# Kernel tuning notes

Hardware: AMD Instinct MI355X
Metric: run time of the kernel (lower is better)

## Reference

```python
import jax, jax.numpy as jnp
import numpy as np

WSCALE = 0.05  # keep ReLU MLP activations in a sane range


def setup_inputs() -> dict:
    key = jax.random.key(0)
    ks = jax.random.split(key, 9)
    B, D, H = 2048, 64, 512
    return {
        "x": jax.random.normal(ks[0], (B, D), dtype=jnp.float32),
        "W1": jax.random.normal(ks[1], (H, D), dtype=jnp.float32) * WSCALE,
        "b1": jax.random.normal(ks[2], (H,), dtype=jnp.float32) * WSCALE,
        "W2": jax.random.normal(ks[3], (H, H), dtype=jnp.float32) * WSCALE,
        "b2": jax.random.normal(ks[4], (H,), dtype=jnp.float32) * WSCALE,
        "W3": jax.random.normal(ks[5], (H, H), dtype=jnp.float32) * WSCALE,
        "b3": jax.random.normal(ks[6], (H,), dtype=jnp.float32) * WSCALE,
        "W4": jax.random.normal(ks[7], (D, H), dtype=jnp.float32) * WSCALE,
        "b4": jax.random.normal(ks[8], (D,), dtype=jnp.float32) * WSCALE,
    }


def reference(x, W1, b1, W2, b2, W3, b3, W4, b4):
    # Score network: ReLU MLP (weights stored PyTorch-style [out, in]).
    a1 = x @ W1.T + b1          # [B, H]
    h1 = jax.nn.relu(a1)
    a2 = h1 @ W2.T + b2
    h2 = jax.nn.relu(a2)
    a3 = h2 @ W3.T + b3
    h3 = jax.nn.relu(a3)
    s = h3 @ W4.T + b4          # [B, D] score

    # Divergence = trace of Jacobian ds/dx per sample.
    # Per-sample J = W4 @ diag(m3) @ W3 @ diag(m2) @ W2 @ diag(m1) @ W1,
    # with m_k = 1[a_k > 0] (ReLU derivative; 0 at 0 like torch autograd).
    m1 = (a1 > 0).astype(x.dtype)
    m2 = (a2 > 0).astype(x.dtype)
    m3 = (a3 > 0).astype(x.dtype)
    T = m1[:, :, None] * W1[None, :, :]                 # [B, H, D]
    T = m2[:, :, None] * jnp.einsum('ij,bjd->bid', W2, T)  # [B, H, D]
    T = m3[:, :, None] * jnp.einsum('ij,bjd->bid', W3, T)  # [B, H, D]
    div = jnp.einsum('dj,bjd->b', W4, T)                # trace of J, [B]

    # Hyvarinen score: 0.5 * ||s||^2 + div
    val = 0.5 * jnp.sum(s * s, axis=1) + div
    return val
```

## Files before the change

kernel.cpp:

```cpp
#include <hip/hip_runtime.h>
#include <stdint.h>


typedef __attribute__((ext_vector_type(8))) short short8;
typedef __attribute__((ext_vector_type(4))) float f32x4;

union U16x8 {
  uint4 u;
  short8 s;
};

__device__ __forceinline__ uint16_t f2bf(float f) {
  uint32_t u = __float_as_uint(f);
  uint32_t lsb = (u >> 16) & 1u;
  u += 0x7FFFu + lsb;
  return (uint16_t)(u >> 16);
}

__device__ __forceinline__ void lds_load16(const uint4* gsrc, uint4* ldst) {
  __builtin_amdgcn_global_load_lds(
      (const __attribute__((address_space(1))) void*)gsrc,
      (__attribute__((address_space(3))) void*)ldst, 16, 0, 0);
}

__global__ __launch_bounds__(256) void convert_kernel(
    const float* __restrict__ W1, const float* __restrict__ W2,
    const float* __restrict__ W3, const float* __restrict__ W4,
    uint16_t* __restrict__ A2swz, uint16_t* __restrict__ A3swz,
    uint16_t* __restrict__ B1swz, uint16_t* __restrict__ B4swz,
    float* __restrict__ W2Tf, float* __restrict__ W3Tf,
    float* __restrict__ W1Tf, float* __restrict__ W4Tf) {
  const int i = blockIdx.x * 256 + threadIdx.x;
  if (i < 262144) {
    const int e = i;
    const int f = e >> 3, j = e & 7;
    const int lane = f & 63, fk = f >> 6;
    const int kc = fk & 15, r16 = fk >> 4;
    const int l15 = lane & 15, quad = lane >> 4;
    const int row = r16 * 16 + l15, col = kc * 32 + quad * 8 + j;
    A2swz[e] = f2bf(W2[row * 512 + col]);
  } else if (i < 524288) {
    const int e = i - 262144;
    const int f = e >> 3, j = e & 7;
    const int lane = f & 63, fk = f >> 6;
    const int kc = fk & 15, r16 = fk >> 4;
    const int l15 = lane & 15, quad = lane >> 4;
    const int row = r16 * 16 + l15, col = kc * 32 + quad * 8 + j;
    A3swz[e] = f2bf(W3[col * 512 + row]);
  } else if (i < 557056) {
    const int e = i - 524288;
    const int f = e >> 3, j = e & 7;
    const int lane = f & 63, fk = f >> 6;
    const int kc = fk >> 2, jt = fk & 3;
    const int l15 = lane & 15, quad = lane >> 4;
    const int d = jt * 16 + l15, col = kc * 32 + quad * 8 + j;
    B1swz[e] = f2bf(W1[col * 64 + d]);
  } else if (i < 589824) {
    const int e = i - 557056;
    const int f = e >> 3, j = e & 7;
    const int lane = f & 63, fk = f >> 6;
    const int kc = fk >> 2, jt = fk & 3;
    const int l15 = lane & 15, quad = lane >> 4;
    const int d = jt * 16 + l15, col = kc * 32 + quad * 8 + j;
    B4swz[e] = f2bf(W4[d * 512 + col]);
  } else if (i < 851968) {
    const int e = i - 589824;
    const int k = e >> 9, jj = e & 511;
    W2Tf[e] = W2[jj * 512 + k];
  } else if (i < 1114112) {
    const int e = i - 851968;
    const int k = e >> 9, jj = e & 511;
    W3Tf[e] = W3[jj * 512 + k];
  } else if (i < 1146880) {
    const int e = i - 1114112;
    const int k = e >> 9, jj = e & 511;
    W1Tf[e] = W1[jj * 64 + k];
  } else if (i < 1179648) {
    const int e = i - 1146880;
    const int k = e >> 6, d = e & 63;
    W4Tf[e] = W4[d * 512 + k];
  }
}

__device__ __forceinline__ void relu_store_mask4(
    float acc[4], float (*hdst)[4], uint32_t* __restrict__ mbase,
    int t, int lane, int wv) {
#pragma unroll
  for (int s = 0; s < 4; ++s) {
    const unsigned long long bal = __ballot(acc[s] > 0.f);
    if (lane == 0) {
      uint2 w2;
      w2.x = (uint32_t)bal;
      w2.y = (uint32_t)(bal >> 32);
      *(uint2*)(mbase + (size_t)s * 16 + 2 * wv) = w2;
    }
  }
  float4 r;
  r.x = acc[0] > 0.f ? acc[0] : 0.f;
  r.y = acc[1] > 0.f ? acc[1] : 0.f;
  r.z = acc[2] > 0.f ? acc[2] : 0.f;
  r.w = acc[3] > 0.f ? acc[3] : 0.f;
  *(float4*)&hdst[t][0] = r;
}

__device__ __forceinline__ void fwd_layer(
    const float* __restrict__ WT, const float* __restrict__ bias,
    const float (* __restrict__ src)[4], float (* __restrict__ dst)[4],
    uint32_t* __restrict__ mbase, int t, int lane, int wv, int K) {
  float acc[4];
  {
    const float bj = bias[t];
    acc[0] = bj; acc[1] = bj; acc[2] = bj; acc[3] = bj;
  }
  const float* Wp = WT + t;
  float wA[8], wB[8];
#pragma unroll
  for (int j = 0; j < 8; ++j) wA[j] = Wp[(size_t)j * 512];
#pragma unroll 1
  for (int kb = 0; kb < K; kb += 16) {
#pragma unroll
    for (int j = 0; j < 8; ++j) wB[j] = Wp[(size_t)(kb + 8 + j) * 512];
#pragma unroll
    for (int j = 0; j < 8; ++j) {
      const float4 h = *(const float4*)&src[kb + j][0];
      const float w = wA[j];
      acc[0] = fmaf(w, h.x, acc[0]); acc[1] = fmaf(w, h.y, acc[1]);
      acc[2] = fmaf(w, h.z, acc[2]); acc[3] = fmaf(w, h.w, acc[3]);
    }
    if (kb + 16 < K) {
#pragma unroll
      for (int j = 0; j < 8; ++j) wA[j] = Wp[(size_t)(kb + 16 + j) * 512];
    }
#pragma unroll
    for (int j = 0; j < 8; ++j) {
      const float4 h = *(const float4*)&src[kb + 8 + j][0];
      const float w = wB[j];
      acc[0] = fmaf(w, h.x, acc[0]); acc[1] = fmaf(w, h.y, acc[1]);
      acc[2] = fmaf(w, h.z, acc[2]); acc[3] = fmaf(w, h.w, acc[3]);
    }
  }
  relu_store_mask4(acc, dst, mbase, t, lane, wv);
}

__global__ __launch_bounds__(512) void forward_kernel(
    const float* __restrict__ x,
    const float* __restrict__ W1Tf, const float* __restrict__ b1,
    const float* __restrict__ W2Tf, const float* __restrict__ b2,
    const float* __restrict__ W3Tf, const float* __restrict__ b3,
    const float* __restrict__ W4Tf, const float* __restrict__ b4,
    uint32_t* __restrict__ m1p, uint32_t* __restrict__ m2p,
    uint32_t* __restrict__ m3p, float* __restrict__ out) {
  __shared__ float xs[64][4];
  __shared__ float hA[512][4];
  __shared__ float hB[512][4];
  __shared__ float p4[4][2][64];
  const int t = threadIdx.x;
  const int lane = t & 63, wv = t >> 6;
  const int b0 = blockIdx.x * 4;

  if (t < 256) {
    const int k = t >> 2, s = t & 3;
    xs[k][s] = x[(size_t)(b0 + s) * 64 + k];
  }
  __syncthreads();

  fwd_layer(W1Tf, b1, xs, hA, m1p + (size_t)b0 * 16, t, lane, wv, 64);
  __syncthreads();
  fwd_layer(W2Tf, b2, hA, hB, m2p + (size_t)b0 * 16, t, lane, wv, 512);
  __syncthreads();
  fwd_layer(W3Tf, b3, hB, hA, m3p + (size_t)b0 * 16, t, lane, wv, 512);
  __syncthreads();

  {
    const int s = wv & 3, hh = wv >> 2, d = lane;
    const int k0 = hh * 256;
    const float* Wp = W4Tf + (size_t)k0 * 64 + d;
    float ap[4] = {0.f, 0.f, 0.f, 0.f};
    float wA[8], wB[8];
#pragma unroll
    for (int j = 0; j < 8; ++j) wA[j] = Wp[(size_t)j * 64];
#pragma unroll 1
    for (int kb = 0; kb < 256; kb += 16) {
#pragma unroll
      for (int j = 0; j < 8; ++j) wB[j] = Wp[(size_t)(kb + 8 + j) * 64];
#pragma unroll
      for (int j = 0; j < 8; ++j)
        ap[j & 3] = fmaf(wA[j], hA[k0 + kb + j][s], ap[j & 3]);
      if (kb + 16 < 256) {
#pragma unroll
        for (int j = 0; j < 8; ++j) wA[j] = Wp[(size_t)(kb + 16 + j) * 64];
      }
#pragma unroll
      for (int j = 0; j < 8; ++j)
        ap[j & 3] = fmaf(wB[j], hA[k0 + kb + 8 + j][s], ap[j & 3]);
    }
    p4[s][hh][d] = (ap[0] + ap[1]) + (ap[2] + ap[3]);
  }
  __syncthreads();
  if (wv < 4) {
    const int s = wv, d = lane;
    const float a4 = p4[s][0][d] + p4[s][1][d] + b4[d];
    float sq = a4 * a4;
#pragma unroll
    for (int off = 32; off; off >>= 1) sq += __shfl_down(sq, off, 64);
    if (lane == 0) out[b0 + s] = 0.5f * sq;
  }
}

__device__ __forceinline__ void expand_mask(uint32_t byte8, uint32_t mk[4]) {
#pragma unroll
  for (int i = 0; i < 4; ++i) {
    mk[i] = (((byte8 >> (2 * i)) & 1u) ? 0x0000FFFFu : 0u) |
            (((byte8 >> (2 * i + 1)) & 1u) ? 0xFFFF0000u : 0u);
  }
}

__global__ __launch_bounds__(256, 2) void div_kernel(
    const uint4* __restrict__ A2swz, const uint4* __restrict__ A3swz,
    const uint4* __restrict__ B1swz, const uint4* __restrict__ B4swz,
    const uint32_t* __restrict__ m1p, const uint32_t* __restrict__ m2p,
    const uint32_t* __restrict__ m3p, float* __restrict__ out) {
  __shared__ uint4 sfrag[3][16][64];
  __shared__ uint32_t smask[4][2][16];
  const int t = threadIdx.x;
  const int lane = t & 63, wv = t >> 6;
  const int quad = lane >> 4;
  const int g4 = blockIdx.x;
  const int rowB0 = blockIdx.y * 64;
  const int b = g4 * 4 + wv;
  const int r16b = blockIdx.y * 4;

  const uint4* sb = (wv == 0) ? A2swz : (wv == 1) ? A3swz : (wv == 2) ? B1swz : B4swz;

  f32x4 accC[4][4], accG[4][4];
#pragma unroll
  for (int it = 0; it < 4; ++it)
#pragma unroll
    for (int jt = 0; jt < 4; ++jt) {
      accC[it][jt] = (f32x4){0.f, 0.f, 0.f, 0.f};
      accG[it][jt] = (f32x4){0.f, 0.f, 0.f, 0.f};
    }

  {
    const uint32_t* m1w = m1p + (size_t)b * 16;
    const uint32_t* m3w = m3p + (size_t)b * 16;
    if (lane < 16) smask[wv][0][lane] = m1w[lane];
    else if (lane < 32) smask[wv][1][lane & 15] = m3w[lane & 15];
  }

  auto stage = [&](int sbuf, int kc) {
#pragma unroll
    for (int q = 0; q < 4; ++q) {
      const size_t off = (wv < 2)
          ? ((size_t)((r16b + q) * 16 + kc) * 64 + lane)
          : ((size_t)(kc * 4 + q) * 64 + lane);
      lds_load16(sb + off, &sfrag[sbuf][wv * 4 + q][0]);
    }
  };

  stage(0, 0);
  stage(1, 1);
  __builtin_amdgcn_sched_barrier(0);
  asm volatile("s_waitcnt vmcnt(4)" ::: "memory");
  __builtin_amdgcn_s_barrier();
  __builtin_amdgcn_sched_barrier(0);

#pragma unroll 1
  for (int kc = 0; kc < 16; ++kc) {
    const int rb = kc % 3;
    if (kc < 14) stage((kc + 2) % 3, kc + 2);

    {
      const uint32_t m1d = __builtin_amdgcn_readfirstlane(smask[wv][0][kc]);
      uint32_t mk1[4];
      expand_mask((m1d >> (quad * 8)) & 0xFFu, mk1);

      uint4 a2[4], u1[4];
#pragma unroll
      for (int q = 0; q < 4; ++q) {
        a2[q] = sfrag[rb][q][lane];
        u1[q] = sfrag[rb][8 + q][lane];
      }
      short8 bC[4];
#pragma unroll
      for (int jt = 0; jt < 4; ++jt) {
        U16x8 u;
        u.u = u1[jt];
        u.u.x &= mk1[0]; u.u.y &= mk1[1]; u.u.z &= mk1[2]; u.u.w &= mk1[3];
        bC[jt] = u.s;
      }
      __builtin_amdgcn_s_setprio(1);
#pragma unroll
      for (int it = 0; it < 4; ++it) {
        U16x8 ua;
        ua.u = a2[it];
        const short8 af = ua.s;
#pragma unroll
        for (int jt = 0; jt < 4; ++jt)
          accC[it][jt] = __builtin_amdgcn_mfma_f32_16x16x32_bf16(af, bC[jt], accC[it][jt], 0, 0, 0);
      }
      __builtin_amdgcn_s_setprio(0);
    }

    {
      const uint32_t m3d = __builtin_amdgcn_readfirstlane(smask[wv][1][kc]);
      uint32_t mk3[4];
      expand_mask((m3d >> (quad * 8)) & 0xFFu, mk3);

      uint4 a3[4], u4[4];
#pragma unroll
      for (int q = 0; q < 4; ++q) {
        a3[q] = sfrag[rb][4 + q][lane];
        u4[q] = sfrag[rb][12 + q][lane];
      }
      short8 bG[4];
#pragma unroll
      for (int jt = 0; jt < 4; ++jt) {
        U16x8 u;
        u.u = u4[jt];
        u.u.x &= mk3[0]; u.u.y &= mk3[1]; u.u.z &= mk3[2]; u.u.w &= mk3[3];
        bG[jt] = u.s;
      }
      __builtin_amdgcn_s_setprio(1);
#pragma unroll
      for (int it = 0; it < 4; ++it) {
        U16x8 ua;
        ua.u = a3[it];
        const short8 af = ua.s;
#pragma unroll
        for (int jt = 0; jt < 4; ++jt)
          accG[it][jt] = __builtin_amdgcn_mfma_f32_16x16x32_bf16(af, bG[jt], accG[it][jt], 0, 0, 0);
      }
      __builtin_amdgcn_s_setprio(0);
    }

    if (kc < 14) {
      asm volatile("s_waitcnt vmcnt(4)" ::: "memory");
    } else if (kc == 14) {
      asm volatile("s_waitcnt vmcnt(0)" ::: "memory");
    }
    if (kc < 15) {
      __builtin_amdgcn_s_barrier();
      __builtin_amdgcn_sched_barrier(0);
    }
  }

  const uint32_t* m2w = m2p + (size_t)b * 16;
  float dsum = 0.f;
#pragma unroll
  for (int it = 0; it < 4; ++it) {
    const int rloc = it * 16 + quad * 4;
    const uint32_t md = m2w[(rowB0 + rloc) >> 5];
    const uint32_t bits = (md >> (rloc & 31)) & 0xFu;
    const float w0 = (bits & 1u) ? 1.f : 0.f;
    const float w1 = (bits & 2u) ? 1.f : 0.f;
    const float w2 = (bits & 4u) ? 1.f : 0.f;
    const float w3 = (bits & 8u) ? 1.f : 0.f;
#pragma unroll
    for (int jt = 0; jt < 4; ++jt) {
      dsum = fmaf(w0, accC[it][jt][0] * accG[it][jt][0], dsum);
      dsum = fmaf(w1, accC[it][jt][1] * accG[it][jt][1], dsum);
      dsum = fmaf(w2, accC[it][jt][2] * accG[it][jt][2], dsum);
      dsum = fmaf(w3, accC[it][jt][3] * accG[it][jt][3], dsum);
    }
  }
#pragma unroll
  for (int off = 32; off; off >>= 1) dsum += __shfl_down(dsum, off, 64);
  if (lane == 0) atomicAdd(out + b, dsum);
}

extern "C" void kernel_launch(void* const* d_in, const int* in_sizes, int n_in,
                              void* d_out, int out_size, void* d_ws, size_t ws_size,
                              hipStream_t stream) {
  const float* x  = (const float*)d_in[0];
  const float* W1 = (const float*)d_in[1];
  const float* b1 = (const float*)d_in[2];
  const float* W2 = (const float*)d_in[3];
  const float* b2 = (const float*)d_in[4];
  const float* W3 = (const float*)d_in[5];
  const float* b3 = (const float*)d_in[6];
  const float* W4 = (const float*)d_in[7];
  const float* b4 = (const float*)d_in[8];
  float* out = (float*)d_out;

  char* ws = (char*)d_ws;
  uint16_t* A2swz = (uint16_t*)(ws + 0);
  uint16_t* A3swz = (uint16_t*)(ws + 524288);
  uint16_t* B1swz = (uint16_t*)(ws + 1048576);
  uint16_t* B4swz = (uint16_t*)(ws + 1114112);
  float*    W2Tf  = (float*)(ws + 1179648);
  float*    W3Tf  = (float*)(ws + 2228224);
  float*    W1Tf  = (float*)(ws + 3276800);
  float*    W4Tf  = (float*)(ws + 3407872);
  uint32_t* m1p   = (uint32_t*)(ws + 3538944);
  uint32_t* m2p   = (uint32_t*)(ws + 3670016);
  uint32_t* m3p   = (uint32_t*)(ws + 3801088);
  if (ws_size < 3932160) return;

  convert_kernel<<<4608, 256, 0, stream>>>(W1, W2, W3, W4,
                                           A2swz, A3swz, B1swz, B4swz,
                                           W2Tf, W3Tf, W1Tf, W4Tf);
  forward_kernel<<<512, 512, 0, stream>>>(x, W1Tf, b1, W2Tf, b2, W3Tf, b3,
                                          W4Tf, b4, m1p, m2p, m3p, out);
  div_kernel<<<dim3(512, 8), 256, 0, stream>>>((const uint4*)A2swz,
                                               (const uint4*)A3swz,
                                               (const uint4*)B1swz,
                                               (const uint4*)B4swz,
                                               m1p, m2p, m3p, out);
}
```

Measured before the change: 280.0 us.

## Split C and G products across separate waves with LDS exchange in div kernel

The divergence kernel now runs 8 waves per block instead of 4. Half the waves compute the C accumulators and the other half compute the G accumulators, which halves the accumulator registers per wave and allows higher occupancy. Mask expansion is precomputed into LDS once, so the inner loop no longer expands masks each iteration. The C results pass to the G waves through LDS in two halves for the final masked dot product, which adds extra barriers and LDS traffic in the epilogue.

```diff
diff --git a/kernel.cpp b/kernel.cpp
--- a/kernel.cpp
+++ b/kernel.cpp
@@ -215,127 +215,96 @@
   }
 }
 
-__global__ __launch_bounds__(256, 2) void div_kernel(
+__global__ __launch_bounds__(512, 4) void div_kernel(
     const uint4* __restrict__ A2swz, const uint4* __restrict__ A3swz,
     const uint4* __restrict__ B1swz, const uint4* __restrict__ B4swz,
     const uint32_t* __restrict__ m1p, const uint32_t* __restrict__ m2p,
     const uint32_t* __restrict__ m3p, float* __restrict__ out) {
   __shared__ uint4 sfrag[3][16][64];
-  __shared__ uint32_t smask[4][2][16];
+  __shared__ uint4 emask[8][16][4];
   const int t = threadIdx.x;
   const int lane = t & 63, wv = t >> 6;
-  const int quad = lane >> 4;
+  const int quad = lane >> 4, l15 = lane & 15;
   const int g4 = blockIdx.x;
   const int rowB0 = blockIdx.y * 64;
-  const int b = g4 * 4 + wv;
+  const int sLoc = wv & 3;
+  const int b = g4 * 4 + sLoc;
   const int r16b = blockIdx.y * 4;
-
-  const uint4* sb = (wv == 0) ? A2swz : (wv == 1) ? A3swz : (wv == 2) ? B1swz : B4swz;
-
-  f32x4 accC[4][4], accG[4][4];
+  const bool isC = (wv < 4);
+
+  const uint4* sb = (wv < 2) ? A2swz : (wv < 4) ? B1swz : (wv < 6) ? A3swz : B4swz;
+
+  f32x4 acc[4][4];
 #pragma unroll
   for (int it = 0; it < 4; ++it)
 #pragma unroll
-    for (int jt = 0; jt < 4; ++jt) {
-      accC[it][jt] = (f32x4){0.f, 0.f, 0.f, 0.f};
-      accG[it][jt] = (f32x4){0.f, 0.f, 0.f, 0.f};
-    }
+    for (int jt = 0; jt < 4; ++jt) acc[it][jt] = (f32x4){0.f, 0.f, 0.f, 0.f};
 
   {
-    const uint32_t* m1w = m1p + (size_t)b * 16;
-    const uint32_t* m3w = m3p + (size_t)b * 16;
-    if (lane < 16) smask[wv][0][lane] = m1w[lane];
-    else if (lane < 32) smask[wv][1][lane & 15] = m3w[lane & 15];
+    const uint32_t* mp = (isC ? m1p : m3p) + (size_t)b * 16;
+    const int kcl = lane >> 2, qd = lane & 3;
+    const uint32_t word = mp[kcl];
+    uint32_t mk[4];
+    expand_mask((word >> (qd * 8)) & 0xFFu, mk);
+    uint4 v;
+    v.x = mk[0]; v.y = mk[1]; v.z = mk[2]; v.w = mk[3];
+    emask[wv][kcl][qd] = v;
   }
 
   auto stage = [&](int sbuf, int kc) {
 #pragma unroll
-    for (int q = 0; q < 4; ++q) {
-      const size_t off = (wv < 2)
-          ? ((size_t)((r16b + q) * 16 + kc) * 64 + lane)
-          : ((size_t)(kc * 4 + q) * 64 + lane);
-      lds_load16(sb + off, &sfrag[sbuf][wv * 4 + q][0]);
+    for (int q = 0; q < 2; ++q) {
+      const int sub = (wv & 1) * 2 + q;
+      const size_t off = ((wv & 2) == 0)
+          ? ((size_t)((r16b + sub) * 16 + kc) * 64 + lane)
+          : ((size_t)(kc * 4 + sub) * 64 + lane);
+      lds_load16(sb + off, &sfrag[sbuf][wv * 2 + q][0]);
     }
   };
 
   stage(0, 0);
   stage(1, 1);
   __builtin_amdgcn_sched_barrier(0);
-  asm volatile("s_waitcnt vmcnt(4)" ::: "memory");
+  asm volatile("s_waitcnt vmcnt(2)" ::: "memory");
   __builtin_amdgcn_s_barrier();
   __builtin_amdgcn_sched_barrier(0);
+
+  const int base = isC ? 0 : 8;
 
 #pragma unroll 1
   for (int kc = 0; kc < 16; ++kc) {
     const int rb = kc % 3;
     if (kc < 14) stage((kc + 2) % 3, kc + 2);
 
-    {
-      const uint32_t m1d = __builtin_amdgcn_readfirstlane(smask[wv][0][kc]);
-      uint32_t mk1[4];
-      expand_mask((m1d >> (quad * 8)) & 0xFFu, mk1);
-
-      uint4 a2[4], u1[4];
-#pragma unroll
-      for (int q = 0; q < 4; ++q) {
-        a2[q] = sfrag[rb][q][lane];
-        u1[q] = sfrag[rb][8 + q][lane];
-      }
-      short8 bC[4];
-#pragma unroll
-      for (int jt = 0; jt < 4; ++jt) {
-        U16x8 u;
-        u.u = u1[jt];
-        u.u.x &= mk1[0]; u.u.y &= mk1[1]; u.u.z &= mk1[2]; u.u.w &= mk1[3];
-        bC[jt] = u.s;
-      }
-      __builtin_amdgcn_s_setprio(1);
-#pragma unroll
-      for (int it = 0; it < 4; ++it) {
-        U16x8 ua;
-        ua.u = a2[it];
-        const short8 af = ua.s;
-#pragma unroll
-        for (int jt = 0; jt < 4; ++jt)
-          accC[it][jt] = __builtin_amdgcn_mfma_f32_16x16x32_bf16(af, bC[jt], accC[it][jt], 0, 0, 0);
-      }
-      __builtin_amdgcn_s_setprio(0);
-    }
-
-    {
-      const uint32_t m3d = __builtin_amdgcn_readfirstlane(smask[wv][1][kc]);
-      uint32_t mk3[4];
-      expand_mask((m3d >> (quad * 8)) & 0xFFu, mk3);
-
-      uint4 a3[4], u4[4];
-#pragma unroll
-      for (int q = 0; q < 4; ++q) {
-        a3[q] = sfrag[rb][4 + q][lane];
-        u4[q] = sfrag[rb][12 + q][lane];
-      }
-      short8 bG[4];
-#pragma unroll
-      for (int jt = 0; jt < 4; ++jt) {
-        U16x8 u;
-        u.u = u4[jt];
-        u.u.x &= mk3[0]; u.u.y &= mk3[1]; u.u.z &= mk3[2]; u.u.w &= mk3[3];
-        bG[jt] = u.s;
-      }
-      __builtin_amdgcn_s_setprio(1);
-#pragma unroll
-      for (int it = 0; it < 4; ++it) {
-        U16x8 ua;
-        ua.u = a3[it];
-        const short8 af = ua.s;
-#pragma unroll
-        for (int jt = 0; jt < 4; ++jt)
-          accG[it][jt] = __builtin_amdgcn_mfma_f32_16x16x32_bf16(af, bG[jt], accG[it][jt], 0, 0, 0);
-      }
-      __builtin_amdgcn_s_setprio(0);
+    const uint4 mku = emask[wv][kc][quad];
+
+    uint4 a[4], u[4];
+#pragma unroll
+    for (int q = 0; q < 4; ++q) {
+      a[q] = sfrag[rb][base + q][lane];
+      u[q] = sfrag[rb][base + 4 + q][lane];
+    }
+
+    short8 bf[4];
+#pragma unroll
+    for (int jt = 0; jt < 4; ++jt) {
+      U16x8 uu;
+      uu.u = u[jt];
+      uu.u.x &= mku.x; uu.u.y &= mku.y; uu.u.z &= mku.z; uu.u.w &= mku.w;
+      bf[jt] = uu.s;
+    }
+#pragma unroll
+    for (int it = 0; it < 4; ++it) {
+      U16x8 ua;
+      ua.u = a[it];
+      const short8 af = ua.s;
+#pragma unroll
+      for (int jt = 0; jt < 4; ++jt)
+        acc[it][jt] = __builtin_amdgcn_mfma_f32_16x16x32_bf16(af, bf[jt], acc[it][jt], 0, 0, 0);
     }
 
     if (kc < 14) {
-      asm volatile("s_waitcnt vmcnt(4)" ::: "memory");
+      asm volatile("s_waitcnt vmcnt(2)" ::: "memory");
     } else if (kc == 14) {
       asm volatile("s_waitcnt vmcnt(0)" ::: "memory");
     }
@@ -345,28 +314,55 @@
     }
   }
 
+  __syncthreads();
+  float* cxf = (float*)&sfrag[0][0][0];
+  float dsum = 0.f;
   const uint32_t* m2w = m2p + (size_t)b * 16;
-  float dsum = 0.f;
-#pragma unroll
-  for (int it = 0; it < 4; ++it) {
-    const int rloc = it * 16 + quad * 4;
-    const uint32_t md = m2w[(rowB0 + rloc) >> 5];
-    const uint32_t bits = (md >> (rloc & 31)) & 0xFu;
-    const float w0 = (bits & 1u) ? 1.f : 0.f;
-    const float w1 = (bits & 2u) ? 1.f : 0.f;
-    const float w2 = (bits & 4u) ? 1.f : 0.f;
-    const float w3 = (bits & 8u) ? 1.f : 0.f;
-#pragma unroll
-    for (int jt = 0; jt < 4; ++jt) {
-      dsum = fmaf(w0, accC[it][jt][0] * accG[it][jt][0], dsum);
-      dsum = fmaf(w1, accC[it][jt][1] * accG[it][jt][1], dsum);
-      dsum = fmaf(w2, accC[it][jt][2] * accG[it][jt][2], dsum);
-      dsum = fmaf(w3, accC[it][jt][3] * accG[it][jt][3], dsum);
-    }
-  }
-#pragma unroll
-  for (int off = 32; off; off >>= 1) dsum += __shfl_down(dsum, off, 64);
-  if (lane == 0) atomicAdd(out + b, dsum);
+#pragma unroll
+  for (int h = 0; h < 2; ++h) {
+    if (isC) {
+#pragma unroll
+      for (int ith = 0; ith < 2; ++ith)
+#pragma unroll
+        for (int jt = 0; jt < 4; ++jt) {
+          float* crow = &cxf[((size_t)sLoc * 32 + ith * 16 + quad * 4) * 65 +
+                             jt * 16 + l15];
+          crow[0 * 65] = acc[h * 2 + ith][jt][0];
+          crow[1 * 65] = acc[h * 2 + ith][jt][1];
+          crow[2 * 65] = acc[h * 2 + ith][jt][2];
+          crow[3 * 65] = acc[h * 2 + ith][jt][3];
+        }
+    }
+    __syncthreads();
+    if (!isC) {
+#pragma unroll
+      for (int ith = 0; ith < 2; ++ith) {
+        const int it = h * 2 + ith;
+        const int rloc = it * 16 + quad * 4;
+        const uint32_t md = m2w[(rowB0 + rloc) >> 5];
+        const uint32_t bits = (md >> (rloc & 31)) & 0xFu;
+        const float w0 = (bits & 1u) ? 1.f : 0.f;
+        const float w1 = (bits & 2u) ? 1.f : 0.f;
+        const float w2 = (bits & 4u) ? 1.f : 0.f;
+        const float w3 = (bits & 8u) ? 1.f : 0.f;
+#pragma unroll
+        for (int jt = 0; jt < 4; ++jt) {
+          const float* crow = &cxf[((size_t)sLoc * 32 + ith * 16 + quad * 4) * 65 +
+                                   jt * 16 + l15];
+          dsum = fmaf(w0, acc[it][jt][0] * crow[0 * 65], dsum);
+          dsum = fmaf(w1, acc[it][jt][1] * crow[1 * 65], dsum);
+          dsum = fmaf(w2, acc[it][jt][2] * crow[2 * 65], dsum);
+          dsum = fmaf(w3, acc[it][jt][3] * crow[3 * 65], dsum);
+        }
+      }
+    }
+    __syncthreads();
+  }
+  if (!isC) {
+#pragma unroll
+    for (int off = 32; off; off >>= 1) dsum += __shfl_down(dsum, off, 64);
+    if (lane == 0) atomicAdd(out + b, dsum);
+  }
 }
 
 extern "C" void kernel_launch(void* const* d_in, const int* in_sizes, int n_in,
@@ -402,7 +398,7 @@
                                            W2Tf, W3Tf, W1Tf, W4Tf);
   forward_kernel<<<512, 512, 0, stream>>>(x, W1Tf, b1, W2Tf, b2, W3Tf, b3,
                                           W4Tf, b4, m1p, m2p, m3p, out);
-  div_kernel<<<dim3(512, 8), 256, 0, stream>>>((const uint4*)A2swz,
+  div_kernel<<<dim3(512, 8), 512, 0, stream>>>((const uint4*)A2swz,
                                                (const uint4*)A3swz,
                                                (const uint4*)B1swz,
                                                (const uint4*)B4swz,
```

Result: faster. 266.0 us (-5.0%).
